# Kernel optimization log

Measured on AMD Instinct MI355X. Metric: run time of the kernel, lower is better.

## Reference

```python
import jax, jax.numpy as jnp
import numpy as np

MODEL_DIM = 1024
FF_DIMS = (1024, 2048, 4096)  # max_ff_dim // 2**(num_levels-1-level), floored at model_dim
NUM_LEVELS = 3


def _gelu(x):
    return jax.nn.gelu(x, approximate=False)  # torch nn.GELU default is exact erf GELU


def setup_inputs() -> dict:
    key = jax.random.key(0)
    ks = jax.random.split(key, 20)
    d = MODEL_DIM
    inp = {
        "token_embeddings": jax.random.normal(ks[0], (4, 4096, d), dtype=jnp.float32),
        # importance classifier: Linear(d, d//2) -> GELU -> Linear(d//2, num_levels) -> Softmax
        "Wc1": jax.random.normal(ks[1], (d, d // 2), dtype=jnp.float32) * 0.02,
        "bc1": jnp.zeros((d // 2,), dtype=jnp.float32),
        "Wc2": jax.random.normal(ks[2], (d // 2, NUM_LEVELS), dtype=jnp.float32) * 0.02,
        "bc2": jnp.zeros((NUM_LEVELS,), dtype=jnp.float32),
    }
    # per-level FFN: Linear(d, ff) -> GELU -> Linear(ff, d)
    for lvl, ff in enumerate(FF_DIMS):
        inp[f"W1_{lvl}"] = jax.random.normal(ks[3 + 4 * lvl], (d, ff), dtype=jnp.float32) * 0.02
        inp[f"b1_{lvl}"] = jnp.zeros((ff,), dtype=jnp.float32)
        inp[f"W2_{lvl}"] = jax.random.normal(ks[4 + 4 * lvl], (ff, d), dtype=jnp.float32) * 0.02
        inp[f"b2_{lvl}"] = jnp.zeros((d,), dtype=jnp.float32)
    return inp


def reference(token_embeddings, Wc1, bc1, Wc2, bc2,
              W1_0, b1_0, W2_0, b2_0,
              W1_1, b1_1, W2_1, b2_1,
              W1_2, b1_2, W2_2, b2_2):
    x = token_embeddings  # [B, S, D]
    # importance classifier -> per-token routing level (argmax over softmax probs)
    logits = _gelu(x @ Wc1 + bc1) @ Wc2 + bc2  # [B, S, L]
    probs = jax.nn.softmax(logits, axis=-1)
    levels = jnp.argmax(probs, axis=-1)  # [B, S] int
    # per-level FFN; select per-token output (dense compute + masked select is the
    # jit-friendly equivalent of the gather->MLP->scatter in the original)
    params = ((W1_0, b1_0, W2_0, b2_0), (W1_1, b1_1, W2_1, b2_1), (W1_2, b1_2, W2_2, b2_2))
    out = jnp.zeros_like(x)
    for lvl, (W1, b1, W2, b2) in enumerate(params):
        y = _gelu(x @ W1 + b1) @ W2 + b2  # [B, S, D]
        out = jnp.where((levels == lvl)[..., None], y, out)
    return out
```

## Files before the change

### kernel.cpp

```cpp
#include <hip/hip_runtime.h>
#include <math.h>

#define T_TOTAL 16384
#define DMODEL  1024
#define MARGIN  2.5e-3f

typedef __attribute__((ext_vector_type(8))) _Float16 f16x8;
typedef __attribute__((ext_vector_type(4))) float    f32x4;

#define SEL3(l, a, b, c) ((l) == 0 ? (a) : (l) == 1 ? (b) : (c))

#define CTR_STRIDE 32

__device__ __forceinline__ float gelu_exact(float x) {
    return 0.5f * x * (1.0f + erff(x * 0.7071067811865476f));
}
__device__ __forceinline__ unsigned short f2h(float f) {
    union { _Float16 h; unsigned short s; } c; c.h = (_Float16)f; return c.s;
}
__device__ __forceinline__ float h2f(unsigned short u) {
    union { unsigned short s; _Float16 h; } c; c.s = u; return (float)c.h;
}
__device__ __forceinline__ void gll16(const void* g, void* l) {
    __builtin_amdgcn_global_load_lds(
        (const __attribute__((address_space(1))) unsigned int*)g,
        (__attribute__((address_space(3))) unsigned int*)l, 16, 0, 0);
}

__device__ __forceinline__ int swz_bid() {
    const int b = blockIdx.x;
    const int G = gridDim.x;
    if (G & 63) return b;
    const int x = b & 7, j = b >> 3;
    return (x + 8 * (j >> 3)) * 8 + (j & 7);
}

__global__ __launch_bounds__(256) void k_cvt(
    const float* __restrict__ X, unsigned short* __restrict__ Xh)
{
    const size_t i = ((size_t)blockIdx.x * 256 + threadIdx.x) * 8;
    float4 f0 = *(const float4*)(X + i);
    float4 f1 = *(const float4*)(X + i + 4);
    unsigned short o[8] __attribute__((aligned(16)));
    o[0]=f2h(f0.x); o[1]=f2h(f0.y); o[2]=f2h(f0.z); o[3]=f2h(f0.w);
    o[4]=f2h(f1.x); o[5]=f2h(f1.y); o[6]=f2h(f1.z); o[7]=f2h(f1.w);
    *(uint4*)(Xh + i) = *(uint4*)o;
}

struct PackP {
    const float* src[7];
    unsigned short* dst[7];
    int K[7], N[7];
    int boff[8];
};

__global__ __launch_bounds__(256) void k_pack_all(PackP p)
{
    const int gb = blockIdx.x;
    int t = 0;
    while (t < 6 && gb >= p.boff[t + 1]) ++t;
    const int lb = gb - p.boff[t];
    const float* src = p.src[t];
    unsigned short* dst = p.dst[t];
    const int K = p.K[t], N = p.N[t];

    const int ktiles = K >> 5;
    const int nt = lb / ktiles;
    const int kt = lb % ktiles;
    __shared__ float ls[32][129];
    const int tid = threadIdx.x;
    {
        const int c  = tid >> 3;
        const int n0 = (tid & 7) * 16;
        const float* s = src + (size_t)(kt * 32 + c) * N + (size_t)nt * 128 + n0;
#pragma unroll
        for (int v = 0; v < 4; ++v) {
            float4 f = *(const float4*)(s + v * 4);
            ls[c][n0 + v*4 + 0] = f.x; ls[c][n0 + v*4 + 1] = f.y;
            ls[c][n0 + v*4 + 2] = f.z; ls[c][n0 + v*4 + 3] = f.w;
        }
    }
    __syncthreads();
    {
        const int r  = tid >> 1;
        const int c0 = (tid & 1) * 16;
        unsigned short tmp[16] __attribute__((aligned(16)));
#pragma unroll
        for (int c = 0; c < 16; ++c) tmp[c] = f2h(ls[c0 + c][r]);
        unsigned short* d = dst + (size_t)lb * (128 * 32) + r * 32 + c0;
        *(uint4*)(d)     = *(uint4*)&tmp[0];
        *(uint4*)(d + 8) = *(uint4*)&tmp[8];
    }
}

__global__ __launch_bounds__(256) void k_h(
    const unsigned short* __restrict__ Xh, const unsigned short* __restrict__ Wq,
    const float* __restrict__ bc1, unsigned short* __restrict__ H)
{
    const int bid = swz_bid();
    const int mt = bid >> 2;
    const int nt = bid & 3;
    __shared__ __align__(16) unsigned short As[128 * 32];
    __shared__ __align__(16) unsigned short Bs[128 * 32];

    const int tid = threadIdx.x;
    const int w = tid >> 6, ln = tid & 63;
    const int wr = w >> 1, wc = w & 1;
    const int q = ln >> 4, tq = ln & 15;

    f32x4 acc[4][4];
#pragma unroll
    for (int i = 0; i < 4; ++i)
#pragma unroll
        for (int j = 0; j < 4; ++j) acc[i][j] = (f32x4){0.f, 0.f, 0.f, 0.f};

    const int r0 = mt * 128 + w * 32 + (ln >> 2);
    const unsigned short* a0 = Xh + (size_t)r0 * DMODEL + (ln & 3) * 8;
    const unsigned short* a1 = a0 + (size_t)16 * DMODEL;
    const unsigned short* bsr = Wq + (size_t)nt * 32 * 4096 + w * 1024 + ln * 8;
    unsigned short* lA = As + w * 1024;
    unsigned short* lB = Bs + w * 1024;

    for (int kt = 0; kt < 32; ++kt) {
        __syncthreads();
        gll16(a0 + kt * 32, lA);
        gll16(a1 + kt * 32, lA + 512);
        gll16(bsr + (size_t)kt * 4096,       lB);
        gll16(bsr + (size_t)kt * 4096 + 512, lB + 512);
        __syncthreads();
        f16x8 a[4], b[4];
#pragma unroll
        for (int i = 0; i < 4; ++i) a[i] = *(const f16x8*)(As + (wr*64 + i*16 + tq) * 32 + q * 8);
#pragma unroll
        for (int j = 0; j < 4; ++j) b[j] = *(const f16x8*)(Bs + (wc*64 + j*16 + tq) * 32 + q * 8);
#pragma unroll
        for (int i = 0; i < 4; ++i)
#pragma unroll
            for (int j = 0; j < 4; ++j)
                acc[i][j] = __builtin_amdgcn_mfma_f32_16x16x32_f16(b[j], a[i], acc[i][j], 0, 0, 0);
    }
#pragma unroll
    for (int i = 0; i < 4; ++i) {
        const int t = mt * 128 + wr * 64 + i * 16 + tq;
        unsigned short* hrow = H + (size_t)t * 512;
#pragma unroll
        for (int j = 0; j < 4; ++j) {
            const int cb = nt * 128 + wc * 64 + j * 16 + q * 4;
            float4 bv = *(const float4*)(bc1 + cb);
            f32x4 v = acc[i][j];
            unsigned short o[4] __attribute__((aligned(8)));
            o[0] = f2h(gelu_exact(v[0] + bv.x));
            o[1] = f2h(gelu_exact(v[1] + bv.y));
            o[2] = f2h(gelu_exact(v[2] + bv.z));
            o[3] = f2h(gelu_exact(v[3] + bv.w));
            *(uint2*)(hrow + cb) = *(uint2*)o;
        }
    }
}

__global__ __launch_bounds__(256) void k_levels(
    const unsigned short* __restrict__ H, const float* __restrict__ Wc2,
    const float* __restrict__ bc2, int* __restrict__ ctrs,
    int* __restrict__ idxb, int* __restrict__ flaglist)
{
    __shared__ int lvlbuf[64];
    const int tid  = threadIdx.x;
    const int wv   = tid >> 6, lane = tid & 63;
    const int t0   = blockIdx.x * 64;
    const int j0   = lane * 8;

    float wa[8], wb[8], wc[8];
#pragma unroll
    for (int jj = 0; jj < 8; ++jj) {
        const float* wr = Wc2 + (j0 + jj) * 3;
        wa[jj] = wr[0]; wb[jj] = wr[1]; wc[jj] = wr[2];
    }
    const float bz0 = bc2[0], bz1 = bc2[1], bz2 = bc2[2];

    for (int it = 0; it < 16; ++it) {
        const int t = t0 + wv * 16 + it;
        const unsigned short* hrow = H + (size_t)t * 512 + j0;
        unsigned short hu[8] __attribute__((aligned(16)));
        *(uint4*)hu = *(const uint4*)hrow;

        float a0 = 0.f, a1 = 0.f, a2 = 0.f;
#pragma unroll
        for (int jj = 0; jj < 8; ++jj) {
            const float h = h2f(hu[jj]);
            a0 += h * wa[jj]; a1 += h * wb[jj]; a2 += h * wc[jj];
        }
#pragma unroll
        for (int off = 32; off; off >>= 1) {
            a0 += __shfl_xor(a0, off);
            a1 += __shfl_xor(a1, off);
            a2 += __shfl_xor(a2, off);
        }
        if (lane == 0) {
            a0 += bz0; a1 += bz1; a2 += bz2;
            int lvl = 0; float best = a0;
            if (a1 > best) { best = a1; lvl = 1; }
            if (a2 > best) { best = a2; lvl = 2; }
            float second = (lvl == 0) ? fmaxf(a1, a2) : (lvl == 1) ? fmaxf(a0, a2) : fmaxf(a0, a1);
            lvlbuf[wv * 16 + it] = (best - second < MARGIN) ? 3 : lvl;
        }
    }
    __syncthreads();
    if (tid < 64) {
        const int mylvl = lvlbuf[tid];
        const int mytok = t0 + tid;
#pragma unroll
        for (int lvl = 0; lvl < 4; ++lvl) {
            const unsigned long long m = __ballot(mylvl == lvl);
            int base = 0;
            if (tid == 0) {
                const int cnt = __popcll(m);
                if (cnt) base = atomicAdd(&ctrs[lvl * CTR_STRIDE], cnt);
            }
            base = __shfl(base, 0);
            if (mylvl == lvl) {
                const int pos = base + __popcll(m & ((1ull << tid) - 1ull));
                if (lvl < 3) idxb[lvl * T_TOTAL + pos] = mytok;
                else         flaglist[pos] = mytok;
            }
        }
    }
}

__global__ __launch_bounds__(256) void k_exact(
    const float* __restrict__ X, const float* __restrict__ Wc1,
    const float* __restrict__ bc1, const float* __restrict__ Wc2,
    const float* __restrict__ bc2, const int* __restrict__ flaglist,
    const int* __restrict__ flagcnt, int* __restrict__ ctrs,
    int* __restrict__ idxb)
{
    __shared__ float xs[1024][8];
    __shared__ float red[4][8][3];
    const int tid = threadIdx.x;
    const int nflag = flagcnt[0];

    for (int g = blockIdx.x; g * 8 < nflag; g += gridDim.x) {
        {
            const int s   = tid >> 5;
            const int l32 = tid & 31;
            int fi = g * 8 + s; if (fi >= nflag) fi = nflag - 1;
            const float* xr = X + (size_t)flaglist[fi] * DMODEL;
#pragma unroll
            for (int kk = 0; kk < 32; ++kk) {
                const int k = kk * 32 + l32;
                xs[k][s] = xr[k];
            }
        }
        __syncthreads();
        const int j = tid;
        float acc0[8], acc1[8];
#pragma unroll
        for (int s = 0; s < 8; ++s) { acc0[s] = 0.f; acc1[s] = 0.f; }
        for (int k = 0; k < 1024; ++k) {
            float4 xa = *(const float4*)&xs[k][0];
            float4 xb = *(const float4*)&xs[k][4];
            const float w0 = Wc1[(size_t)k * 512 + j];
            const float w1 = Wc1[(size_t)k * 512 + j + 256];
            acc0[0] += xa.x * w0; acc0[1] += xa.y * w0; acc0[2] += xa.z * w0; acc0[3] += xa.w * w0;
            acc0[4] += xb.x * w0; acc0[5] += xb.y * w0; acc0[6] += xb.z * w0; acc0[7] += xb.w * w0;
            acc1[0] += xa.x * w1; acc1[1] += xa.y * w1; acc1[2] += xa.z * w1; acc1[3] += xa.w * w1;
            acc1[4] += xb.x * w1; acc1[5] += xb.y * w1; acc1[6] += xb.z * w1; acc1[7] += xb.w * w1;
        }
        float p[8][3];
        {
            const float b0 = bc1[j], b1 = bc1[j + 256];
            const float* w2a = Wc2 + j * 3;
            const float* w2b = Wc2 + (j + 256) * 3;
#pragma unroll
            for (int s = 0; s < 8; ++s) {
                const float h0 = gelu_exact(acc0[s] + b0);
                const float h1 = gelu_exact(acc1[s] + b1);
                p[s][0] = h0 * w2a[0] + h1 * w2b[0];
                p[s][1] = h0 * w2a[1] + h1 * w2b[1];
                p[s][2] = h0 * w2a[2] + h1 * w2b[2];
            }
        }
#pragma unroll
        for (int off = 32; off; off >>= 1)
#pragma unroll
            for (int s = 0; s < 8; ++s) {
                p[s][0] += __shfl_xor(p[s][0], off);
                p[s][1] += __shfl_xor(p[s][1], off);
                p[s][2] += __shfl_xor(p[s][2], off);
            }
        if ((tid & 63) == 0) {
            const int w = tid >> 6;
#pragma unroll
            for (int s = 0; s < 8; ++s) {
                red[w][s][0] = p[s][0]; red[w][s][1] = p[s][1]; red[w][s][2] = p[s][2];
            }
        }
        __syncthreads();
        if (tid < 8) {
            const int fi = g * 8 + tid;
            if (fi < nflag) {
                float l0 = bc2[0], l1 = bc2[1], l2 = bc2[2];
#pragma unroll
                for (int w = 0; w < 4; ++w) {
                    l0 += red[w][tid][0]; l1 += red[w][tid][1]; l2 += red[w][tid][2];
                }
                int lvl = 0; float best = l0;
                if (l1 > best) { best = l1; lvl = 1; }
                if (l2 > best) { best = l2; lvl = 2; }
                const int tok = flaglist[fi];
                const int pos = atomicAdd(&ctrs[lvl * CTR_STRIDE], 1);
                idxb[lvl * T_TOTAL + pos] = tok;
            }
        }
        __syncthreads();
    }
}

__global__ void k_offsets(const int* __restrict__ ctrs, int* __restrict__ off,
                          int h0, int h1, int h2)
{
    if (threadIdx.x == 0 && blockIdx.x == 0) {
        off[0] = 0;
        off[1] = ctrs[0] * h0;
        off[2] = ctrs[0] * h0 + ctrs[CTR_STRIDE] * h1;
    }
}

struct FfnP1 {
    const unsigned short *Wq0, *Wq1, *Wq2;
    const float *bb0, *bb1, *bb2;
    const int* counts; const int* off; const int* idx;
    int s0, s01;
    int NT0, NT1, NT2;
    int st0, st1, st2;
    int no0;
};

__global__ __launch_bounds__(256) void k_ffn1(
    const unsigned short* __restrict__ Xh, unsigned short* __restrict__ Hmid, FfnP1 p)
{
    const int bid = swz_bid();
    int l, r;
    if (bid < p.s0)       { l = 0; r = bid; }
    else if (bid < p.s01) { l = 1; r = bid - p.s0; }
    else                  { l = 2; r = bid - p.s01; }
    const int NT = SEL3(l, p.NT0, p.NT1, p.NT2);
    const int mt = r / NT, nt = r % NT;
    const int n  = p.counts[l * CTR_STRIDE];
    if (mt * 128 >= n) return;

    const int* idx = p.idx + l * T_TOTAL;
    const unsigned short* Wq = SEL3(l, p.Wq0, p.Wq1, p.Wq2);
    const float* bb = SEL3(l, p.bb0, p.bb1, p.bb2);
    const int stride = SEL3(l, p.st0, p.st1, p.st2);
    const size_t hoff = (size_t)p.off[l];

    __shared__ __align__(16) unsigned short As[128 * 32];
    __shared__ __align__(16) unsigned short Bs[128 * 32];

    const int tid = threadIdx.x;
    const int w = tid >> 6, ln = tid & 63;
    const int wr = w >> 1, wc = w & 1;
    const int q = ln >> 4, tq = ln & 15;

    f32x4 acc[4][4];
#pragma unroll
    for (int i = 0; i < 4; ++i)
#pragma unroll
        for (int j = 0; j < 4; ++j) acc[i][j] = (f32x4){0.f, 0.f, 0.f, 0.f};

    int r0 = mt * 128 + w * 32 + (ln >> 2);
    int r1 = r0 + 16;
    if (r0 >= n) r0 = n - 1;
    if (r1 >= n) r1 = n - 1;
    const unsigned short* a0 = Xh + (size_t)idx[r0] * DMODEL + (ln & 3) * 8;
    const unsigned short* a1 = Xh + (size_t)idx[r1] * DMODEL + (ln & 3) * 8;
    const unsigned short* bsr = Wq + (size_t)(p.no0 + nt) * 32 * 4096 + w * 1024 + ln * 8;
    unsigned short* lA = As + w * 1024;
    unsigned short* lB = Bs + w * 1024;

    for (int kt = 0; kt < 32; ++kt) {
        __syncthreads();
        gll16(a0 + kt * 32, lA);
        gll16(a1 + kt * 32, lA + 512);
        gll16(bsr + (size_t)kt * 4096,       lB);
        gll16(bsr + (size_t)kt * 4096 + 512, lB + 512);
        __syncthreads();
        f16x8 a[4], b[4];
#pragma unroll
        for (int i = 0; i < 4; ++i) a[i] = *(const f16x8*)(As + (wr*64 + i*16 + tq) * 32 + q * 8);
#pragma unroll
        for (int j = 0; j < 4; ++j) b[j] = *(const f16x8*)(Bs + (wc*64 + j*16 + tq) * 32 + q * 8);
#pragma unroll
        for (int i = 0; i < 4; ++i)
#pragma unroll
            for (int j = 0; j < 4; ++j)
                acc[i][j] = __builtin_amdgcn_mfma_f32_16x16x32_f16(b[j], a[i], acc[i][j], 0, 0, 0);
    }
#pragma unroll
    for (int i = 0; i < 4; ++i) {
        const int pp = mt * 128 + wr * 64 + i * 16 + tq;
        if (pp < n) {
            unsigned short* hrow = Hmid + hoff + (size_t)pp * stride;
#pragma unroll
            for (int j = 0; j < 4; ++j) {
                const int cb = nt * 128 + wc * 64 + j * 16 + q * 4;
                float4 bv = *(const float4*)(bb + p.no0 * 128 + cb);
                f32x4 v = acc[i][j];
                unsigned short o[4] __attribute__((aligned(8)));
                o[0] = f2h(gelu_exact(v[0] + bv.x));
                o[1] = f2h(gelu_exact(v[1] + bv.y));
                o[2] = f2h(gelu_exact(v[2] + bv.z));
                o[3] = f2h(gelu_exact(v[3] + bv.w));
                *(uint2*)(hrow + cb) = *(uint2*)o;
            }
        }
    }
}

struct FfnP2 {
    const unsigned short *Wq0, *Wq1, *Wq2;
    const float *bb0, *bb1, *bb2;
    const int* counts; const int* off; const int* idx;
    int s2, s21;
    int st0, st1, st2;
    int kb;
    int kc0, kc1, kc2;
    int nf0, nf1, nf2;
    int accum;
};

__global__ __launch_bounds__(256) void k_ffn2(
    const unsigned short* __restrict__ Hmid, float* __restrict__ out, FfnP2 p)
{
    const int bid = swz_bid();
    int l, r;
    if (bid < p.s2)       { l = 2; r = bid; }
    else if (bid < p.s21) { l = 1; r = bid - p.s2; }
    else                  { l = 0; r = bid - p.s21; }
    const int mt = r >> 3, nt = r & 7;
    const int n  = p.counts[l * CTR_STRIDE];
    if (mt * 128 >= n) return;

    const int* idx = p.idx + l * T_TOTAL;
    const unsigned short* Wq = SEL3(l, p.Wq0, p.Wq1, p.Wq2);
    const float* bb = SEL3(l, p.bb0, p.bb1, p.bb2);
    const int stride = SEL3(l, p.st0, p.st1, p.st2);
    const int KC = SEL3(l, p.kc0, p.kc1, p.kc2);
    const int nf = SEL3(l, p.nf0, p.nf1, p.nf2);
    const size_t hoff = (size_t)p.off[l];

    __shared__ __align__(16) unsigned short As[128 * 32];
    __shared__ __align__(16) unsigned short Bs[128 * 32];

    const int tid = threadIdx.x;
    const int w = tid >> 6, ln = tid & 63;
    const int wr = w >> 1, wc = w & 1;
    const int q = ln >> 4, tq = ln & 15;

    f32x4 acc[4][4];
#pragma unroll
    for (int i = 0; i < 4; ++i)
#pragma unroll
        for (int j = 0; j < 4; ++j) acc[i][j] = (f32x4){0.f, 0.f, 0.f, 0.f};

    int r0 = mt * 128 + w * 32 + (ln >> 2);
    int r1 = r0 + 16;
    if (r0 >= n) r0 = n - 1;
    if (r1 >= n) r1 = n - 1;
    const unsigned short* a0 = Hmid + hoff + (size_t)r0 * stride + (ln & 3) * 8;
    const unsigned short* a1 = Hmid + hoff + (size_t)r1 * stride + (ln & 3) * 8;
    const unsigned short* bsr = Wq + ((size_t)nt * nf + p.kb) * 4096 + w * 1024 + ln * 8;
    unsigned short* lA = As + w * 1024;
    unsigned short* lB = Bs + w * 1024;

    for (int kt = 0; kt < KC; ++kt) {
        __syncthreads();
        gll16(a0 + kt * 32, lA);
        gll16(a1 + kt * 32, lA + 512);
        gll16(bsr + (size_t)kt * 4096,       lB);
        gll16(bsr + (size_t)kt * 4096 + 512, lB + 512);
        __syncthreads();
        f16x8 a[4], b[4];
#pragma unroll
        for (int i = 0; i < 4; ++i) a[i] = *(const f16x8*)(As + (wr*64 + i*16 + tq) * 32 + q * 8);
#pragma unroll
        for (int j = 0; j < 4; ++j) b[j] = *(const f16x8*)(Bs + (wc*64 + j*16 + tq) * 32 + q * 8);
#pragma unroll
        for (int i = 0; i < 4; ++i)
#pragma unroll
            for (int j = 0; j < 4; ++j)
                acc[i][j] = __builtin_amdgcn_mfma_f32_16x16x32_f16(b[j], a[i], acc[i][j], 0, 0, 0);
    }
#pragma unroll
    for (int i = 0; i < 4; ++i) {
        const int pp = mt * 128 + wr * 64 + i * 16 + tq;
        if (pp < n) {
            float* orow = out + (size_t)idx[pp] * DMODEL;
#pragma unroll
            for (int j = 0; j < 4; ++j) {
                const int cb = nt * 128 + wc * 64 + j * 16 + q * 4;
                f32x4 v = acc[i][j];
                float4 res;
                if (p.accum) {
                    float4 cur = *(const float4*)(orow + cb);
                    res.x = cur.x + v[0]; res.y = cur.y + v[1];
                    res.z = cur.z + v[2]; res.w = cur.w + v[3];
                } else {
                    float4 bv = *(const float4*)(bb + cb);
                    res.x = v[0] + bv.x; res.y = v[1] + bv.y;
                    res.z = v[2] + bv.z; res.w = v[3] + bv.w;
                }
                *(float4*)(orow + cb) = res;
            }
        }
    }
}

extern "C" void kernel_launch(void* const* d_in, const int* in_sizes, int n_in,
                              void* d_out, int out_size, void* d_ws, size_t ws_size,
                              hipStream_t stream)
{
    (void)in_sizes; (void)n_in; (void)out_size;

    const float* X   = (const float*)d_in[0];
    const float* Wc1 = (const float*)d_in[1];
    const float* bc1 = (const float*)d_in[2];
    const float* Wc2 = (const float*)d_in[3];
    const float* bc2 = (const float*)d_in[4];
    const float* W1[3] = {(const float*)d_in[5],  (const float*)d_in[9],  (const float*)d_in[13]};
    const float* b1[3] = {(const float*)d_in[6],  (const float*)d_in[10], (const float*)d_in[14]};
    const float* W2[3] = {(const float*)d_in[7],  (const float*)d_in[11], (const float*)d_in[15]};
    const float* b2[3] = {(const float*)d_in[8],  (const float*)d_in[12], (const float*)d_in[16]};
    float* out = (float*)d_out;
    const int FF[3] = {1024, 2048, 4096};

    char* w = (char*)d_ws;
    size_t o = 0;
    auto take = [&](size_t bytes) -> char* {
        char* p = w + o;
        o = (o + bytes + 255) & ~(size_t)255;
        return p;
    };
    unsigned short* W1p[3]; for (int l = 0; l < 3; ++l) W1p[l] = (unsigned short*)take((size_t)1024 * FF[l] * 2);
    unsigned short* W2p[3]; for (int l = 0; l < 3; ++l) W2p[l] = (unsigned short*)take((size_t)1024 * FF[l] * 2);
    unsigned short* Wc1p = (unsigned short*)take((size_t)1024 * 512 * 2);
    unsigned short* Xh   = (unsigned short*)take((size_t)T_TOTAL * DMODEL * 2);
    unsigned short* H    = (unsigned short*)take((size_t)T_TOTAL * 512 * 2);
    int* flaglist = (int*)take((size_t)T_TOTAL * 4);
    int* idxb     = (int*)take((size_t)3 * T_TOTAL * 4);
    int* ctrs     = (int*)take(1024);
    unsigned short* Hmid = (unsigned short*)(w + o);
    const size_t avail = ws_size > o ? ws_size - o : 0;

    int CHUNK = 256;
    const int cand[4] = {4096, 2048, 1024, 512};
    for (int ci = 0; ci < 4; ++ci)
        if ((size_t)T_TOTAL * cand[ci] * 2 <= avail) { CHUNK = cand[ci]; break; }
    int HC[3]; for (int l = 0; l < 3; ++l) HC[l] = FF[l] < CHUNK ? FF[l] : CHUNK;

    k_cvt<<<(T_TOTAL * DMODEL) / (256 * 8), 256, 0, stream>>>(X, Xh);
    {
        PackP pk;
        int ob = 0, slot = 0;
        auto addpk = [&](const float* s, unsigned short* d2, int K, int N) {
            pk.src[slot] = s; pk.dst[slot] = d2; pk.K[slot] = K; pk.N[slot] = N;
            pk.boff[slot] = ob; ob += (N / 128) * (K / 32); ++slot;
        };
        for (int l = 0; l < 3; ++l) addpk(W1[l], W1p[l], 1024, FF[l]);
        for (int l = 0; l < 3; ++l) addpk(W2[l], W2p[l], FF[l], 1024);
        addpk(Wc1, Wc1p, 1024, 512);
        pk.boff[7] = ob;
        k_pack_all<<<ob, 256, 0, stream>>>(pk);
    }

    k_h<<<(T_TOTAL / 128) * 4, 256, 0, stream>>>(Xh, Wc1p, bc1, H);
    hipMemsetAsync(ctrs, 0, 1024, stream);
    k_levels<<<T_TOTAL / 64, 256, 0, stream>>>(H, Wc2, bc2, ctrs, idxb, flaglist);
    k_exact<<<128, 256, 0, stream>>>(X, Wc1, bc1, Wc2, bc2, flaglist, ctrs + 96, ctrs, idxb);
    k_offsets<<<1, 64, 0, stream>>>(ctrs, ctrs + 128, HC[0], HC[1], HC[2]);

    const int nchunks = FF[2] / CHUNK;
    for (int c = 0; c < nchunks; ++c) {
        int NTc[3];
        for (int l = 0; l < 3; ++l) {
            int rem = FF[l] - c * CHUNK;
            NTc[l] = rem > 0 ? (rem < CHUNK ? rem : CHUNK) / 128 : 0;
        }
        const int g1_0 = 128 * NTc[0], g1_1 = 128 * NTc[1], g1_2 = 128 * NTc[2];
        const int G1 = g1_0 + g1_1 + g1_2;
        const int g2_0 = NTc[0] ? 1024 : 0, g2_1 = NTc[1] ? 1024 : 0, g2_2 = NTc[2] ? 1024 : 0;
        const int G2 = g2_0 + g2_1 + g2_2;
        if (G1 == 0) continue;

        FfnP1 p1;
        p1.Wq0 = W1p[0]; p1.Wq1 = W1p[1]; p1.Wq2 = W1p[2];
        p1.bb0 = b1[0];  p1.bb1 = b1[1];  p1.bb2 = b1[2];
        p1.counts = ctrs; p1.off = ctrs + 128; p1.idx = idxb;
        p1.s0 = g1_0; p1.s01 = g1_0 + g1_1;
        p1.NT0 = NTc[0]; p1.NT1 = NTc[1]; p1.NT2 = NTc[2];
        p1.st0 = HC[0]; p1.st1 = HC[1]; p1.st2 = HC[2];
        p1.no0 = c * CHUNK / 128;
        k_ffn1<<<G1, 256, 0, stream>>>(Xh, Hmid, p1);

        FfnP2 p2;
        p2.Wq0 = W2p[0]; p2.Wq1 = W2p[1]; p2.Wq2 = W2p[2];
        p2.bb0 = b2[0];  p2.bb1 = b2[1];  p2.bb2 = b2[2];
        p2.counts = ctrs; p2.off = ctrs + 128; p2.idx = idxb;
        p2.s2 = g2_2; p2.s21 = g2_2 + g2_1;
        p2.st0 = HC[0]; p2.st1 = HC[1]; p2.st2 = HC[2];
        p2.kb = c * CHUNK / 32;
        p2.kc0 = NTc[0] * 4; p2.kc1 = NTc[1] * 4; p2.kc2 = NTc[2] * 4;
        p2.nf0 = FF[0] / 32; p2.nf1 = FF[1] / 32; p2.nf2 = FF[2] / 32;
        p2.accum = (c > 0) ? 1 : 0;
        k_ffn2<<<G2, 256, 0, stream>>>(Hmid, out, p2);
    }
}
```

Baseline: 579.5 us.

## Double-buffer LDS tiles in the three GEMM kernels to overlap loads with MFMA

Each GEMM kernel gets two LDS buffers for the A and B tiles. While the current buffer feeds the MFMA instructions, the global-to-LDS loads for the next k-step are issued into the other buffer, and there is one barrier per iteration instead of two. The goal is to hide global load latency behind compute. LDS use per block doubles to 32 KB, which may lower occupancy, and whether the async global_load_lds writes are properly waited on before the barrier depends on the compiler's waitcnt handling.

Result: no change. 569.5 us (-1.7%).

```diff
diff --git a/kernel.cpp b/kernel.cpp
--- a/kernel.cpp
+++ b/kernel.cpp
@@ -100,8 +100,8 @@
     const int bid = swz_bid();
     const int mt = bid >> 2;
     const int nt = bid & 3;
-    __shared__ __align__(16) unsigned short As[128 * 32];
-    __shared__ __align__(16) unsigned short Bs[128 * 32];
+    __shared__ __align__(16) unsigned short As[2 * 128 * 32];
+    __shared__ __align__(16) unsigned short Bs[2 * 128 * 32];
 
     const int tid = threadIdx.x;
     const int w = tid >> 6, ln = tid & 63;
@@ -118,26 +118,36 @@
     const unsigned short* a0 = Xh + (size_t)r0 * DMODEL + (ln & 3) * 8;
     const unsigned short* a1 = a0 + (size_t)16 * DMODEL;
     const unsigned short* bsr = Wq + (size_t)nt * 32 * 4096 + w * 1024 + ln * 8;
-    unsigned short* lA = As + w * 1024;
-    unsigned short* lB = Bs + w * 1024;
-
+
+    gll16(a0,        As + w * 1024);
+    gll16(a1,        As + w * 1024 + 512);
+    gll16(bsr,       Bs + w * 1024);
+    gll16(bsr + 512, Bs + w * 1024 + 512);
+    __syncthreads();
+
+    int cur = 0;
     for (int kt = 0; kt < 32; ++kt) {
-        __syncthreads();
-        gll16(a0 + kt * 32, lA);
-        gll16(a1 + kt * 32, lA + 512);
-        gll16(bsr + (size_t)kt * 4096,       lB);
-        gll16(bsr + (size_t)kt * 4096 + 512, lB + 512);
-        __syncthreads();
+        const int nxt = cur ^ 1;
+        if (kt + 1 < 32) {
+            gll16(a0 + (kt+1) * 32,                    As + nxt * 4096 + w * 1024);
+            gll16(a1 + (kt+1) * 32,                    As + nxt * 4096 + w * 1024 + 512);
+            gll16(bsr + (size_t)(kt+1) * 4096,         Bs + nxt * 4096 + w * 1024);
+            gll16(bsr + (size_t)(kt+1) * 4096 + 512,   Bs + nxt * 4096 + w * 1024 + 512);
+        }
+        const unsigned short* rA = As + cur * 4096;
+        const unsigned short* rB = Bs + cur * 4096;
         f16x8 a[4], b[4];
 #pragma unroll
-        for (int i = 0; i < 4; ++i) a[i] = *(const f16x8*)(As + (wr*64 + i*16 + tq) * 32 + q * 8);
-#pragma unroll
-        for (int j = 0; j < 4; ++j) b[j] = *(const f16x8*)(Bs + (wc*64 + j*16 + tq) * 32 + q * 8);
+        for (int i = 0; i < 4; ++i) a[i] = *(const f16x8*)(rA + (wr*64 + i*16 + tq) * 32 + q * 8);
+#pragma unroll
+        for (int j = 0; j < 4; ++j) b[j] = *(const f16x8*)(rB + (wc*64 + j*16 + tq) * 32 + q * 8);
 #pragma unroll
         for (int i = 0; i < 4; ++i)
 #pragma unroll
             for (int j = 0; j < 4; ++j)
                 acc[i][j] = __builtin_amdgcn_mfma_f32_16x16x32_f16(b[j], a[i], acc[i][j], 0, 0, 0);
+        __syncthreads();
+        cur = nxt;
     }
 #pragma unroll
     for (int i = 0; i < 4; ++i) {
@@ -354,8 +364,8 @@
     const int stride = SEL3(l, p.st0, p.st1, p.st2);
     const size_t hoff = (size_t)p.off[l];
 
-    __shared__ __align__(16) unsigned short As[128 * 32];
-    __shared__ __align__(16) unsigned short Bs[128 * 32];
+    __shared__ __align__(16) unsigned short As[2 * 128 * 32];
+    __shared__ __align__(16) unsigned short Bs[2 * 128 * 32];
 
     const int tid = threadIdx.x;
     const int w = tid >> 6, ln = tid & 63;
@@ -375,26 +385,36 @@
     const unsigned short* a0 = Xh + (size_t)idx[r0] * DMODEL + (ln & 3) * 8;
     const unsigned short* a1 = Xh + (size_t)idx[r1] * DMODEL + (ln & 3) * 8;
     const unsigned short* bsr = Wq + (size_t)(p.no0 + nt) * 32 * 4096 + w * 1024 + ln * 8;
-    unsigned short* lA = As + w * 1024;
-    unsigned short* lB = Bs + w * 1024;
-
+
+    gll16(a0,        As + w * 1024);
+    gll16(a1,        As + w * 1024 + 512);
+    gll16(bsr,       Bs + w * 1024);
+    gll16(bsr + 512, Bs + w * 1024 + 512);
+    __syncthreads();
+
+    int cur = 0;
     for (int kt = 0; kt < 32; ++kt) {
-        __syncthreads();
-        gll16(a0 + kt * 32, lA);
-        gll16(a1 + kt * 32, lA + 512);
-        gll16(bsr + (size_t)kt * 4096,       lB);
-        gll16(bsr + (size_t)kt * 4096 + 512, lB + 512);
-        __syncthreads();
+        const int nxt = cur ^ 1;
+        if (kt + 1 < 32) {
+            gll16(a0 + (kt+1) * 32,                  As + nxt * 4096 + w * 1024);
+            gll16(a1 + (kt+1) * 32,                  As + nxt * 4096 + w * 1024 + 512);
+            gll16(bsr + (size_t)(kt+1) * 4096,       Bs + nxt * 4096 + w * 1024);
+            gll16(bsr + (size_t)(kt+1) * 4096 + 512, Bs + nxt * 4096 + w * 1024 + 512);
+        }
+        const unsigned short* rA = As + cur * 4096;
+        const unsigned short* rB = Bs + cur * 4096;
         f16x8 a[4], b[4];
 #pragma unroll
-        for (int i = 0; i < 4; ++i) a[i] = *(const f16x8*)(As + (wr*64 + i*16 + tq) * 32 + q * 8);
-#pragma unroll
-        for (int j = 0; j < 4; ++j) b[j] = *(const f16x8*)(Bs + (wc*64 + j*16 + tq) * 32 + q * 8);
+        for (int i = 0; i < 4; ++i) a[i] = *(const f16x8*)(rA + (wr*64 + i*16 + tq) * 32 + q * 8);
+#pragma unroll
+        for (int j = 0; j < 4; ++j) b[j] = *(const f16x8*)(rB + (wc*64 + j*16 + tq) * 32 + q * 8);
 #pragma unroll
         for (int i = 0; i < 4; ++i)
 #pragma unroll
             for (int j = 0; j < 4; ++j)
                 acc[i][j] = __builtin_amdgcn_mfma_f32_16x16x32_f16(b[j], a[i], acc[i][j], 0, 0, 0);
+        __syncthreads();
+        cur = nxt;
     }
 #pragma unroll
     for (int i = 0; i < 4; ++i) {
@@ -449,8 +469,8 @@
     const int nf = SEL3(l, p.nf0, p.nf1, p.nf2);
     const size_t hoff = (size_t)p.off[l];
 
-    __shared__ __align__(16) unsigned short As[128 * 32];
-    __shared__ __align__(16) unsigned short Bs[128 * 32];
+    __shared__ __align__(16) unsigned short As[2 * 128 * 32];
+    __shared__ __align__(16) unsigned short Bs[2 * 128 * 32];
 
     const int tid = threadIdx.x;
     const int w = tid >> 6, ln = tid & 63;
@@ -470,26 +490,36 @@
     const unsigned short* a0 = Hmid + hoff + (size_t)r0 * stride + (ln & 3) * 8;
     const unsigned short* a1 = Hmid + hoff + (size_t)r1 * stride + (ln & 3) * 8;
     const unsigned short* bsr = Wq + ((size_t)nt * nf + p.kb) * 4096 + w * 1024 + ln * 8;
-    unsigned short* lA = As + w * 1024;
-    unsigned short* lB = Bs + w * 1024;
-
+
+    gll16(a0,        As + w * 1024);
+    gll16(a1,        As + w * 1024 + 512);
+    gll16(bsr,       Bs + w * 1024);
+    gll16(bsr + 512, Bs + w * 1024 + 512);
+    __syncthreads();
+
+    int cur = 0;
     for (int kt = 0; kt < KC; ++kt) {
-        __syncthreads();
-        gll16(a0 + kt * 32, lA);
-        gll16(a1 + kt * 32, lA + 512);
-        gll16(bsr + (size_t)kt * 4096,       lB);
-        gll16(bsr + (size_t)kt * 4096 + 512, lB + 512);
-        __syncthreads();
+        const int nxt = cur ^ 1;
+        if (kt + 1 < KC) {
+            gll16(a0 + (kt+1) * 32,                  As + nxt * 4096 + w * 1024);
+            gll16(a1 + (kt+1) * 32,                  As + nxt * 4096 + w * 1024 + 512);
+            gll16(bsr + (size_t)(kt+1) * 4096,       Bs + nxt * 4096 + w * 1024);
+            gll16(bsr + (size_t)(kt+1) * 4096 + 512, Bs + nxt * 4096 + w * 1024 + 512);
+        }
+        const unsigned short* rA = As + cur * 4096;
+        const unsigned short* rB = Bs + cur * 4096;
         f16x8 a[4], b[4];
 #pragma unroll
-        for (int i = 0; i < 4; ++i) a[i] = *(const f16x8*)(As + (wr*64 + i*16 + tq) * 32 + q * 8);
-#pragma unroll
-        for (int j = 0; j < 4; ++j) b[j] = *(const f16x8*)(Bs + (wc*64 + j*16 + tq) * 32 + q * 8);
+        for (int i = 0; i < 4; ++i) a[i] = *(const f16x8*)(rA + (wr*64 + i*16 + tq) * 32 + q * 8);
+#pragma unroll
+        for (int j = 0; j < 4; ++j) b[j] = *(const f16x8*)(rB + (wc*64 + j*16 + tq) * 32 + q * 8);
 #pragma unroll
         for (int i = 0; i < 4; ++i)
 #pragma unroll
             for (int j = 0; j < 4; ++j)
                 acc[i][j] = __builtin_amdgcn_mfma_f32_16x16x32_f16(b[j], a[i], acc[i][j], 0, 0, 0);
+        __syncthreads();
+        cur = nxt;
     }
 #pragma unroll
     for (int i = 0; i < 4; ++i) {
@@ -502,9 +532,9 @@
                 f32x4 v = acc[i][j];
                 float4 res;
                 if (p.accum) {
-                    float4 cur = *(const float4*)(orow + cb);
-                    res.x = cur.x + v[0]; res.y = cur.y + v[1];
-                    res.z = cur.z + v[2]; res.w = cur.w + v[3];
+                    float4 cur4 = *(const float4*)(orow + cb);
+                    res.x = cur4.x + v[0]; res.y = cur4.y + v[1];
+                    res.z = cur4.z + v[2]; res.w = cur4.w + v[3];
                 } else {
                     float4 bv = *(const float4*)(bb + cb);
                     res.x = v[0] + bv.x; res.y = v[1] + bv.y;
```
